# Kernel optimization log

Hardware: AMD Instinct MI355X
Metric: run time of the kernel (lower is better)

Reference implementation:

```python
import jax, jax.numpy as jnp
import numpy as np

N = 50000  # nodes
E = 1600000  # directed edges
F_IN = 64
H = 64
C = 16
EPS = 1e-12


def setup_inputs() -> dict:
    key = jax.random.key(0)
    ks = jax.random.split(key, 10)
    x = jax.random.normal(ks[0], (N, F_IN), jnp.float32)
    edge_index = jax.random.randint(ks[1], (2, E), 0, N, dtype=jnp.int32)
    def lin(k, fan_in, fan_out):
        return jax.random.normal(k, (fan_in, fan_out), jnp.float32) * (1.0 / np.sqrt(fan_in))
    return {
        "x": x,
        "edge_index": edge_index,
        "W1": lin(ks[2], F_IN, H), "b1": jnp.zeros((H,), jnp.float32),
        "W2": lin(ks[3], H, H),    "b2": jnp.zeros((H,), jnp.float32),
        "W3": lin(ks[4], H, H),    "b3": jnp.zeros((H,), jnp.float32),
        "Wlin": lin(ks[5], 3 * H, C), "blin": jnp.zeros((C,), jnp.float32),
    }


def _gcn_norm(edge_index, n):
    # add self loops, compute symmetric GCN normalization D^-1/2 (A+I) D^-1/2
    loop = jnp.arange(n, dtype=edge_index.dtype)
    row = jnp.concatenate([edge_index[0], loop])  # target nodes
    col = jnp.concatenate([edge_index[1], loop])  # source nodes
    deg = jax.ops.segment_sum(jnp.ones_like(row, dtype=jnp.float32), row, num_segments=n)
    dis = jnp.where(deg > 0, jax.lax.rsqrt(jnp.maximum(deg, 1.0)), 0.0)
    norm = dis[row] * dis[col]  # [E+N]
    return row, col, norm


def _gcn_layer(x, row, col, norm, W, b):
    h = x @ W                              # [N, H]
    msg = h[col] * norm[:, None]           # gather sources, scale
    agg = jax.ops.segment_sum(msg, row, num_segments=x.shape[0])  # scatter-add
    return agg + b


def _l2norm(x):
    # torch F.normalize(p=2, dim=1)
    n = jnp.sqrt(jnp.sum(x * x, axis=1, keepdims=True))
    return x / jnp.maximum(n, EPS)


def reference(x, edge_index, W1, b1, W2, b2, W3, b3, Wlin, blin):
    row, col, norm = _gcn_norm(edge_index, x.shape[0])
    stack = []
    h = x
    for (W, b) in ((W1, b1), (W2, b2), (W3, b3)):
        h = _gcn_layer(h, row, col, norm, W, b)
        h = jax.nn.relu(h)
        h = _l2norm(h)
        stack.append(h)
    emb = jnp.concatenate(stack, axis=1)   # [N, 3H]
    out = emb @ Wlin + blin                # [N, C]
    return jax.nn.log_softmax(out, axis=1)
```

## Files before the change

kernel.cpp:

```cpp
#include <hip/hip_runtime.h>
#include <hip/hip_bf16.h>

#define NN 50000
#define EE 1600000
#define NB 391
#define CAPB 4608
#define CPAD 16
#define EPB 4096
#define BCAP 28

typedef __attribute__((ext_vector_type(8))) short short8;
typedef __attribute__((ext_vector_type(4))) float floatx4;

__device__ __forceinline__ float ldext(const void* p, long i, int f32) {
    return f32 ? ((const float*)p)[i]
               : __bfloat162float(((const __hip_bfloat16*)p)[i]);
}

__device__ __forceinline__ float b2f(unsigned short u) {
    unsigned int x = ((unsigned int)u) << 16;
    float f; __builtin_memcpy(&f, &x, 4); return f;
}
__device__ __forceinline__ unsigned short f2b(float f) {
    __hip_bfloat16 h = __float2bfloat16(f);
    unsigned short u; __builtin_memcpy(&u, &h, 2); return u;
}
__device__ __forceinline__ float asf(unsigned int x) {
    float f; __builtin_memcpy(&f, &x, 4); return f;
}

__global__ void k_bucket(const int* __restrict__ row, const int* __restrict__ col,
                         int* __restrict__ bcur, unsigned int* __restrict__ bdata,
                         const unsigned short* __restrict__ xu, int* __restrict__ flag) {
    __shared__ int lcnt[NB];
    __shared__ unsigned binned[NB * BCAP];
    __shared__ int dcnt;
    int tid = threadIdx.x;
    if (blockIdx.x == 0) {
        if (tid == 0) dcnt = 0;
        __syncthreads();
        int local = 0;
        for (int j = 0; j < 16; ++j) {
            unsigned short u = xu[2 * (tid + 256 * j)];
            int ex = (u >> 7) & 0xFF;
            if (ex == 0xFF || ex < 0x60) local++;
        }
        atomicAdd(&dcnt, local);
        __syncthreads();
        if (tid == 0) flag[0] = (dcnt > 256) ? 1 : 0;
    }
    long base = (long)blockIdx.x * EPB;
    int nedge = (int)min((long)EPB, (long)EE - base);
    for (int k = tid; k < NB; k += 256) lcnt[k] = 0;
    __syncthreads();
    const int4* r4 = (const int4*)(row + base);
    const int4* c4 = (const int4*)(col + base);
    for (int j = tid; j < (nedge >> 2); j += 256) {
        int4 rr = r4[j], cc = c4[j];
        #pragma unroll
        for (int t = 0; t < 4; ++t) {
            int r = (&rr.x)[t], c = (&cc.x)[t];
            int b = r >> 7;
            unsigned rec = ((unsigned)(r & 127) << 16) | (unsigned)c;
            int p = atomicAdd(&lcnt[b], 1);
            if (p < BCAP) binned[b * BCAP + p] = rec;
            else {
                int gp = atomicAdd(&bcur[b * CPAD], 1);
                if (gp < CAPB) bdata[(long)b * CAPB + gp] = rec;
            }
        }
    }
    __syncthreads();
    for (int b = tid; b < NB; b += 256) {
        int n = min(lcnt[b], BCAP);
        if (!n) continue;
        int gb = atomicAdd(&bcur[b * CPAD], n);
        long dst = (long)b * CAPB;
        for (int j = 0; j < n; ++j)
            if (gb + j < CAPB) bdata[dst + gb + j] = binned[b * BCAP + j];
    }
}

__global__ void k_csr(const int* __restrict__ bcur, const unsigned* __restrict__ bdata,
                      int* __restrict__ row_ptr, float* __restrict__ dis,
                      unsigned short* __restrict__ csr_col) {
    __shared__ unsigned recs[CAPB];
    __shared__ int cnt[128];
    __shared__ int incl[128];
    __shared__ int curs[128];
    __shared__ int redu[4];
    int b = blockIdx.x, tid = threadIdx.x;
    int lane = tid & 63, wid = tid >> 6;
    int part = 0;
    for (int j = tid; j < b; j += 256) part += min(bcur[j * CPAD], CAPB);
    #pragma unroll
    for (int off = 32; off; off >>= 1) part += __shfl_xor(part, off);
    if (lane == 0) redu[wid] = part;
    if (tid < 128) cnt[tid] = 0;
    __syncthreads();
    int base = redu[0] + redu[1] + redu[2] + redu[3];
    int n = min(bcur[b * CPAD], CAPB);
    const unsigned* dp = bdata + (long)b * CAPB;
    for (int i = tid; i < n; i += 256) {
        unsigned rec = dp[i];
        recs[i] = rec;
        atomicAdd(&cnt[(rec >> 16) & 127], 1);
    }
    __syncthreads();
    if (tid < 128) {
        int x = cnt[tid];
        #pragma unroll
        for (int off = 1; off < 64; off <<= 1) {
            int y = __shfl_up(x, off);
            if (lane >= off) x += y;
        }
        incl[tid] = x;
    }
    __syncthreads();
    int r0 = b << 7;
    if (tid < 128) {
        int ic = incl[tid] + (wid == 1 ? incl[63] : 0);
        int excl = base + ic - cnt[tid];
        curs[tid] = excl;
        int r = r0 + tid;
        if (r <= NN) row_ptr[r] = excl;
        if (r < NN) dis[r] = rsqrtf((float)(cnt[tid] + 1));
    }
    __syncthreads();
    for (int i = tid; i < n; i += 256) {
        unsigned rec = recs[i];
        int p = atomicAdd(&curs[(rec >> 16) & 127], 1);
        csr_col[p] = (unsigned short)(rec & 0xFFFF);
    }
}

template <bool EXT>
__global__ void k_gemm(const void* __restrict__ X, const void* __restrict__ W,
                       const int* __restrict__ flag, const float* __restrict__ dis,
                       unsigned short* __restrict__ Hout) {
    __shared__ __align__(16) unsigned short xs[64 * 72];
    int tid = threadIdx.x;
    int n0 = blockIdx.x * 64;
    const int f32 = flag[0];
    for (int idx = tid; idx < 4096; idx += 256) {
        int nn = idx >> 6, k = idx & 63;
        int n = n0 + nn;
        unsigned short v = 0;
        if (n < NN) {
            long ofs = (long)n * 64 + k;
            if (EXT) v = f32 ? f2b(((const float*)X)[ofs]) : ((const unsigned short*)X)[ofs];
            else     v = ((const unsigned short*)X)[ofs];
        }
        xs[nn * 72 + k] = v;
    }
    __syncthreads();
    int lane = tid & 63, wid = tid >> 6;
    int m0 = wid * 16;
    int quad = lane >> 4, nl = lane & 15;
    short8 a0 = *(const short8*)(xs + (m0 + nl) * 72 + quad * 8);
    short8 a1 = *(const short8*)(xs + (m0 + nl) * 72 + quad * 8 + 32);
    floatx4 acc[4];
    const unsigned short* Wb = (const unsigned short*)W;
    const float* Wf = (const float*)W;
    #pragma unroll
    for (int ct = 0; ct < 4; ++ct) {
        short8 b0, b1;
        int n = ct * 16 + nl;
        #pragma unroll
        for (int j = 0; j < 8; ++j) {
            int k0 = quad * 8 + j;
            b0[j] = (short)(f32 ? f2b(Wf[k0 * 64 + n]) : Wb[k0 * 64 + n]);
            b1[j] = (short)(f32 ? f2b(Wf[(k0 + 32) * 64 + n]) : Wb[(k0 + 32) * 64 + n]);
        }
        floatx4 c = {0.f, 0.f, 0.f, 0.f};
        c = __builtin_amdgcn_mfma_f32_16x16x32_bf16(a0, b0, c, 0, 0, 0);
        c = __builtin_amdgcn_mfma_f32_16x16x32_bf16(a1, b1, c, 0, 0, 0);
        acc[ct] = c;
    }
    #pragma unroll
    for (int r = 0; r < 4; ++r) {
        int node = n0 + m0 + quad * 4 + r;
        if (node < NN) {
            float dn = dis[node];
            #pragma unroll
            for (int ct = 0; ct < 4; ++ct)
                Hout[(long)node * 64 + ct * 16 + nl] = f2b(dn * acc[ct][r]);
        }
    }
}

__global__ void k_agg(const uint4* __restrict__ hp128, const int* __restrict__ row_ptr,
                      const unsigned short* __restrict__ csr_col,
                      const float* __restrict__ dis, const void* __restrict__ bias,
                      const int* __restrict__ flag,
                      unsigned short* __restrict__ eo ) {
    int lane = threadIdx.x & 63, wid = threadIdx.x >> 6;
    int half = lane >> 5;
    int i = blockIdx.x * 8 + wid * 2 + half;
    bool valid = (i < NN);
    int iv = valid ? i : 0;
    int q4 = (lane >> 3) & 3;
    int fl = lane & 7;
    float2 A0 = {0,0}, A1 = {0,0}, A2 = {0,0}, A3 = {0,0};
    #define ADDU(u) do { \
        A0.x += asf((u).x << 16); A0.y += asf((u).x & 0xFFFF0000u); \
        A1.x += asf((u).y << 16); A1.y += asf((u).y & 0xFFFF0000u); \
        A2.x += asf((u).z << 16); A2.y += asf((u).z & 0xFFFF0000u); \
        A3.x += asf((u).w << 16); A3.y += asf((u).w & 0xFFFF0000u); } while (0)
    if (valid && q4 == 0) {
        uint4 u = hp128[(long)iv * 8 + fl];
        ADDU(u);
    }
    int e  = valid ? row_ptr[iv] : 0;
    int e1 = valid ? row_ptr[iv + 1] : 0;
    while (e + 15 < e1) {
        int c0 = csr_col[e + q4];
        int c1 = csr_col[e + 4 + q4];
        int c2 = csr_col[e + 8 + q4];
        int c3 = csr_col[e + 12 + q4];
        uint4 u0 = hp128[(long)c0 * 8 + fl];
        uint4 u1 = hp128[(long)c1 * 8 + fl];
        uint4 u2 = hp128[(long)c2 * 8 + fl];
        uint4 u3 = hp128[(long)c3 * 8 + fl];
        ADDU(u0); ADDU(u1); ADDU(u2); ADDU(u3);
        e += 16;
    }
    if (e + 7 < e1) {
        int c0 = csr_col[e + q4];
        int c1 = csr_col[e + 4 + q4];
        uint4 u0 = hp128[(long)c0 * 8 + fl];
        uint4 u1 = hp128[(long)c1 * 8 + fl];
        ADDU(u0); ADDU(u1);
        e += 8;
    }
    if (e + 3 < e1) {
        int c = csr_col[e + q4];
        uint4 u = hp128[(long)c * 8 + fl];
        ADDU(u);
        e += 4;
    }
    int rem = e1 - e;
    if (q4 < rem) {
        int c = csr_col[e + q4];
        uint4 u = hp128[(long)c * 8 + fl];
        ADDU(u);
    }
    #undef ADDU
    #pragma unroll
    for (int off = 8; off < 32; off <<= 1) {
        A0.x += __shfl_xor(A0.x, off); A0.y += __shfl_xor(A0.y, off);
        A1.x += __shfl_xor(A1.x, off); A1.y += __shfl_xor(A1.y, off);
        A2.x += __shfl_xor(A2.x, off); A2.y += __shfl_xor(A2.y, off);
        A3.x += __shfl_xor(A3.x, off); A3.y += __shfl_xor(A3.y, off);
    }
    const int f32 = flag[0];
    float di = dis[iv];
    float v0 = fmaf(di, A0.x, ldext(bias, 8 * fl + 0, f32));
    float v1 = fmaf(di, A0.y, ldext(bias, 8 * fl + 1, f32));
    float v2 = fmaf(di, A1.x, ldext(bias, 8 * fl + 2, f32));
    float v3 = fmaf(di, A1.y, ldext(bias, 8 * fl + 3, f32));
    float v4 = fmaf(di, A2.x, ldext(bias, 8 * fl + 4, f32));
    float v5 = fmaf(di, A2.y, ldext(bias, 8 * fl + 5, f32));
    float v6 = fmaf(di, A3.x, ldext(bias, 8 * fl + 6, f32));
    float v7 = fmaf(di, A3.y, ldext(bias, 8 * fl + 7, f32));
    v0 = fmaxf(v0, 0.f); v1 = fmaxf(v1, 0.f); v2 = fmaxf(v2, 0.f); v3 = fmaxf(v3, 0.f);
    v4 = fmaxf(v4, 0.f); v5 = fmaxf(v5, 0.f); v6 = fmaxf(v6, 0.f); v7 = fmaxf(v7, 0.f);
    float s = fmaf(v0, v0, fmaf(v1, v1, fmaf(v2, v2, v3 * v3)))
            + fmaf(v4, v4, fmaf(v5, v5, fmaf(v6, v6, v7 * v7)));
    #pragma unroll
    for (int off = 4; off; off >>= 1) s += __shfl_xor(s, off);
    float inv = 1.f / fmaxf(sqrtf(s), 1e-12f);
    if (valid && q4 == 0) {
        union { unsigned short us[8]; uint4 v; } pk;
        pk.us[0] = f2b(v0 * inv); pk.us[1] = f2b(v1 * inv);
        pk.us[2] = f2b(v2 * inv); pk.us[3] = f2b(v3 * inv);
        pk.us[4] = f2b(v4 * inv); pk.us[5] = f2b(v5 * inv);
        pk.us[6] = f2b(v6 * inv); pk.us[7] = f2b(v7 * inv);
        *(uint4*)(eo + (long)i * 64 + 8 * fl) = pk.v;
    }
}

__global__ void k_out(const unsigned short* __restrict__ emb, const void* __restrict__ Wlin,
                      const void* __restrict__ blin, const int* __restrict__ flag,
                      void* __restrict__ out) {
    int tid = threadIdx.x, lane = tid & 63, wid = tid >> 6;
    int quad = lane >> 4, nl = lane & 15;
    int base = blockIdx.x * 64 + wid * 16;
    const int f32 = flag[0];
    const unsigned short* Wb = (const unsigned short*)Wlin;
    const float* Wf = (const float*)Wlin;
    int ia = min(base + nl, NN - 1);
    floatx4 c = {0.f, 0.f, 0.f, 0.f};
    #pragma unroll
    for (int kc = 0; kc < 6; ++kc) {
        short8 b;
        #pragma unroll
        for (int j = 0; j < 8; ++j) {
            int k = kc * 32 + quad * 8 + j;
            b[j] = (short)(f32 ? f2b(Wf[k * 16 + nl]) : Wb[k * 16 + nl]);
        }
        int L = kc >> 1, ko = (kc & 1) * 32 + quad * 8;
        short8 a = *(const short8*)(emb + (long)L * NN * 64 + (long)ia * 64 + ko);
        c = __builtin_amdgcn_mfma_f32_16x16x32_bf16(a, b, c, 0, 0, 0);
    }
    float bl = ldext(blin, nl, f32);
    #pragma unroll
    for (int r = 0; r < 4; ++r) {
        float v = c[r] + bl;
        float m = v;
        #pragma unroll
        for (int off = 1; off < 16; off <<= 1) m = fmaxf(m, __shfl_xor(m, off));
        float ex = __expf(v - m);
        float s = ex;
        #pragma unroll
        for (int off = 1; off < 16; off <<= 1) s += __shfl_xor(s, off);
        float o = (v - m) - __logf(s);
        int node = base + quad * 4 + r;
        if (node < NN) {
            long oidx = (long)node * 16 + nl;
            if (f32) ((float*)out)[oidx] = o;
            else     ((__hip_bfloat16*)out)[oidx] = __float2bfloat16(o);
        }
    }
}

extern "C" void kernel_launch(void* const* d_in, const int* in_sizes, int n_in,
                              void* d_out, int out_size, void* d_ws, size_t ws_size,
                              hipStream_t stream) {
    const void* x    = d_in[0];
    const int*  ei   = (const int*)d_in[1];
    const void* W1   = d_in[2];
    const void* b1   = d_in[3];
    const void* W2   = d_in[4];
    const void* b2   = d_in[5];
    const void* W3   = d_in[6];
    const void* b3   = d_in[7];
    const void* Wlin = d_in[8];
    const void* blin = d_in[9];

    unsigned short* h   = (unsigned short*)d_ws;
    unsigned short* emb = h + (long)NN * 64;
    float* dis     = (float*)(emb + (long)3 * NN * 64);
    int*   row_ptr = (int*)(dis + NN);
    int*   flag    = row_ptr + NN + 64;
    int*   bcur    = flag + 16;
    unsigned* bdata = (unsigned*)(bcur + NB * CPAD);
    unsigned short* csr_col = (unsigned short*)(bdata + (long)NB * CAPB);

    const int* row = ei;
    const int* col = ei + EE;

    (void)hipMemsetAsync(bcur, 0, NB * CPAD * sizeof(int), stream);
    k_bucket<<<(EE + EPB - 1) / EPB, 256, 0, stream>>>(row, col, bcur, bdata,
                                                       (const unsigned short*)x, flag);
    k_csr<<<NB, 256, 0, stream>>>(bcur, bdata, row_ptr, dis, csr_col);

    int gb = (NN + 63) / 64;
    int ga = (NN + 7) / 8;
    const uint4* hp128 = (const uint4*)h;
    k_gemm<true><<<gb, 256, 0, stream>>>(x, W1, flag, dis, h);
    k_agg<<<ga, 256, 0, stream>>>(hp128, row_ptr, csr_col, dis, b1, flag, emb);
    k_gemm<false><<<gb, 256, 0, stream>>>(emb, W2, flag, dis, h);
    k_agg<<<ga, 256, 0, stream>>>(hp128, row_ptr, csr_col, dis, b2, flag, emb + (long)NN * 64);
    k_gemm<false><<<gb, 256, 0, stream>>>(emb + (long)NN * 64, W3, flag, dis, h);
    k_agg<<<ga, 256, 0, stream>>>(hp128, row_ptr, csr_col, dis, b3, flag, emb + (long)2 * NN * 64);

    k_out<<<gb, 256, 0, stream>>>(emb, Wlin, blin, flag, d_out);
}
```

Before: 286.6 us.

## Slice hidden features into 8-column planes and defer L2 normalization downstream

Stores the hidden matrix as eight feature slices of 8 bf16 each, so each aggregation block handles one slice and its gathers touch a 800KB plane that can stay cache-resident, with 32 lanes striding over edges per node. L2 normalization moves out of aggregation: each slice writes its partial sum of squares, and the next GEMM or the output kernel combines them and applies the inverse norm. This cuts the gather working set but multiplies block count by 8 and re-reads row_ptr and csr_col once per slice. It also relies on NN being divisible by 8, since the grid drops the bounds check.

```diff
diff --git a/kernel.cpp b/kernel.cpp
--- a/kernel.cpp
+++ b/kernel.cpp
@@ -135,21 +135,37 @@
 }
 
 template <bool EXT>
-__global__ void k_gemm(const void* __restrict__ X, const void* __restrict__ W,
-                       const int* __restrict__ flag, const float* __restrict__ dis,
-                       unsigned short* __restrict__ Hout) {
+__global__ void k_gemm(const void* __restrict__ X, const float* __restrict__ sqin,
+                       const void* __restrict__ W, const int* __restrict__ flag,
+                       const float* __restrict__ dis,
+                       unsigned short* __restrict__ hs) {
     __shared__ __align__(16) unsigned short xs[64 * 72];
+    __shared__ float inv[64];
     int tid = threadIdx.x;
     int n0 = blockIdx.x * 64;
     const int f32 = flag[0];
+    if (!EXT) {
+        if (tid < 64) {
+            int node = min(n0 + tid, NN - 1);
+            float s8 = 0.f;
+            #pragma unroll
+            for (int s = 0; s < 8; ++s) s8 += sqin[(long)s * NN + node];
+            inv[tid] = 1.f / fmaxf(sqrtf(s8), 1e-12f);
+        }
+        __syncthreads();
+    }
     for (int idx = tid; idx < 4096; idx += 256) {
         int nn = idx >> 6, k = idx & 63;
         int n = n0 + nn;
         unsigned short v = 0;
         if (n < NN) {
-            long ofs = (long)n * 64 + k;
-            if (EXT) v = f32 ? f2b(((const float*)X)[ofs]) : ((const unsigned short*)X)[ofs];
-            else     v = ((const unsigned short*)X)[ofs];
+            if (EXT) {
+                long ofs = (long)n * 64 + k;
+                v = f32 ? f2b(((const float*)X)[ofs]) : ((const unsigned short*)X)[ofs];
+            } else {
+                unsigned short tv = ((const unsigned short*)X)[((long)(k >> 3) * NN + n) * 8 + (k & 7)];
+                v = f2b(b2f(tv) * inv[nn]);
+            }
         }
         xs[nn * 72 + k] = v;
     }
@@ -183,114 +199,91 @@
         if (node < NN) {
             float dn = dis[node];
             #pragma unroll
-            for (int ct = 0; ct < 4; ++ct)
-                Hout[(long)node * 64 + ct * 16 + nl] = f2b(dn * acc[ct][r]);
-        }
-    }
-}
-
-__global__ void k_agg(const uint4* __restrict__ hp128, const int* __restrict__ row_ptr,
+            for (int ct = 0; ct < 4; ++ct) {
+                int slice = 2 * ct + (nl >> 3);
+                hs[((long)slice * NN + node) * 8 + (nl & 7)] = f2b(dn * acc[ct][r]);
+            }
+        }
+    }
+}
+
+__global__ void k_agg(const uint4* __restrict__ hs, const int* __restrict__ row_ptr,
                       const unsigned short* __restrict__ csr_col,
                       const float* __restrict__ dis, const void* __restrict__ bias,
                       const int* __restrict__ flag,
-                      unsigned short* __restrict__ eo ) {
+                      unsigned short* __restrict__ t, float* __restrict__ sq) {
     int lane = threadIdx.x & 63, wid = threadIdx.x >> 6;
-    int half = lane >> 5;
-    int i = blockIdx.x * 8 + wid * 2 + half;
-    bool valid = (i < NN);
-    int iv = valid ? i : 0;
-    int q4 = (lane >> 3) & 3;
-    int fl = lane & 7;
+    int s = blockIdx.x & 7;
+    int half = lane >> 5, el = lane & 31;
+    int i = (blockIdx.x >> 3) * 8 + wid * 2 + half;
+    const uint4* hss = hs + (long)s * NN;
     float2 A0 = {0,0}, A1 = {0,0}, A2 = {0,0}, A3 = {0,0};
     #define ADDU(u) do { \
         A0.x += asf((u).x << 16); A0.y += asf((u).x & 0xFFFF0000u); \
         A1.x += asf((u).y << 16); A1.y += asf((u).y & 0xFFFF0000u); \
         A2.x += asf((u).z << 16); A2.y += asf((u).z & 0xFFFF0000u); \
         A3.x += asf((u).w << 16); A3.y += asf((u).w & 0xFFFF0000u); } while (0)
-    if (valid && q4 == 0) {
-        uint4 u = hp128[(long)iv * 8 + fl];
+    if (el == 0) {
+        uint4 u = hss[i];
         ADDU(u);
     }
-    int e  = valid ? row_ptr[iv] : 0;
-    int e1 = valid ? row_ptr[iv + 1] : 0;
-    while (e + 15 < e1) {
-        int c0 = csr_col[e + q4];
-        int c1 = csr_col[e + 4 + q4];
-        int c2 = csr_col[e + 8 + q4];
-        int c3 = csr_col[e + 12 + q4];
-        uint4 u0 = hp128[(long)c0 * 8 + fl];
-        uint4 u1 = hp128[(long)c1 * 8 + fl];
-        uint4 u2 = hp128[(long)c2 * 8 + fl];
-        uint4 u3 = hp128[(long)c3 * 8 + fl];
-        ADDU(u0); ADDU(u1); ADDU(u2); ADDU(u3);
-        e += 16;
-    }
-    if (e + 7 < e1) {
-        int c0 = csr_col[e + q4];
-        int c1 = csr_col[e + 4 + q4];
-        uint4 u0 = hp128[(long)c0 * 8 + fl];
-        uint4 u1 = hp128[(long)c1 * 8 + fl];
-        ADDU(u0); ADDU(u1);
-        e += 8;
-    }
-    if (e + 3 < e1) {
-        int c = csr_col[e + q4];
-        uint4 u = hp128[(long)c * 8 + fl];
+    int e0 = row_ptr[i], e1 = row_ptr[i + 1];
+    for (int e = e0 + el; e < e1; e += 32) {
+        int c = csr_col[e];
+        uint4 u = hss[c];
         ADDU(u);
-        e += 4;
-    }
-    int rem = e1 - e;
-    if (q4 < rem) {
-        int c = csr_col[e + q4];
-        uint4 u = hp128[(long)c * 8 + fl];
-        ADDU(u);
     }
     #undef ADDU
     #pragma unroll
-    for (int off = 8; off < 32; off <<= 1) {
+    for (int off = 1; off < 32; off <<= 1) {
         A0.x += __shfl_xor(A0.x, off); A0.y += __shfl_xor(A0.y, off);
         A1.x += __shfl_xor(A1.x, off); A1.y += __shfl_xor(A1.y, off);
         A2.x += __shfl_xor(A2.x, off); A2.y += __shfl_xor(A2.y, off);
         A3.x += __shfl_xor(A3.x, off); A3.y += __shfl_xor(A3.y, off);
     }
     const int f32 = flag[0];
-    float di = dis[iv];
-    float v0 = fmaf(di, A0.x, ldext(bias, 8 * fl + 0, f32));
-    float v1 = fmaf(di, A0.y, ldext(bias, 8 * fl + 1, f32));
-    float v2 = fmaf(di, A1.x, ldext(bias, 8 * fl + 2, f32));
-    float v3 = fmaf(di, A1.y, ldext(bias, 8 * fl + 3, f32));
-    float v4 = fmaf(di, A2.x, ldext(bias, 8 * fl + 4, f32));
-    float v5 = fmaf(di, A2.y, ldext(bias, 8 * fl + 5, f32));
-    float v6 = fmaf(di, A3.x, ldext(bias, 8 * fl + 6, f32));
-    float v7 = fmaf(di, A3.y, ldext(bias, 8 * fl + 7, f32));
-    v0 = fmaxf(v0, 0.f); v1 = fmaxf(v1, 0.f); v2 = fmaxf(v2, 0.f); v3 = fmaxf(v3, 0.f);
-    v4 = fmaxf(v4, 0.f); v5 = fmaxf(v5, 0.f); v6 = fmaxf(v6, 0.f); v7 = fmaxf(v7, 0.f);
-    float s = fmaf(v0, v0, fmaf(v1, v1, fmaf(v2, v2, v3 * v3)))
-            + fmaf(v4, v4, fmaf(v5, v5, fmaf(v6, v6, v7 * v7)));
-    #pragma unroll
-    for (int off = 4; off; off >>= 1) s += __shfl_xor(s, off);
-    float inv = 1.f / fmaxf(sqrtf(s), 1e-12f);
-    if (valid && q4 == 0) {
+    float di = dis[i];
+    float v0 = fmaxf(fmaf(di, A0.x, ldext(bias, 8 * s + 0, f32)), 0.f);
+    float v1 = fmaxf(fmaf(di, A0.y, ldext(bias, 8 * s + 1, f32)), 0.f);
+    float v2 = fmaxf(fmaf(di, A1.x, ldext(bias, 8 * s + 2, f32)), 0.f);
+    float v3 = fmaxf(fmaf(di, A1.y, ldext(bias, 8 * s + 3, f32)), 0.f);
+    float v4 = fmaxf(fmaf(di, A2.x, ldext(bias, 8 * s + 4, f32)), 0.f);
+    float v5 = fmaxf(fmaf(di, A2.y, ldext(bias, 8 * s + 5, f32)), 0.f);
+    float v6 = fmaxf(fmaf(di, A3.x, ldext(bias, 8 * s + 6, f32)), 0.f);
+    float v7 = fmaxf(fmaf(di, A3.y, ldext(bias, 8 * s + 7, f32)), 0.f);
+    if (el == 0) {
+        float ss = fmaf(v0, v0, fmaf(v1, v1, fmaf(v2, v2, v3 * v3)))
+                 + fmaf(v4, v4, fmaf(v5, v5, fmaf(v6, v6, v7 * v7)));
         union { unsigned short us[8]; uint4 v; } pk;
-        pk.us[0] = f2b(v0 * inv); pk.us[1] = f2b(v1 * inv);
-        pk.us[2] = f2b(v2 * inv); pk.us[3] = f2b(v3 * inv);
-        pk.us[4] = f2b(v4 * inv); pk.us[5] = f2b(v5 * inv);
-        pk.us[6] = f2b(v6 * inv); pk.us[7] = f2b(v7 * inv);
-        *(uint4*)(eo + (long)i * 64 + 8 * fl) = pk.v;
-    }
-}
-
-__global__ void k_out(const unsigned short* __restrict__ emb, const void* __restrict__ Wlin,
-                      const void* __restrict__ blin, const int* __restrict__ flag,
-                      void* __restrict__ out) {
+        pk.us[0] = f2b(v0); pk.us[1] = f2b(v1); pk.us[2] = f2b(v2); pk.us[3] = f2b(v3);
+        pk.us[4] = f2b(v4); pk.us[5] = f2b(v5); pk.us[6] = f2b(v6); pk.us[7] = f2b(v7);
+        *(uint4*)(t + ((long)s * NN + i) * 8) = pk.v;
+        sq[(long)s * NN + i] = ss;
+    }
+}
+
+__global__ void k_out(const unsigned short* __restrict__ t, const float* __restrict__ sq,
+                      const void* __restrict__ Wlin, const void* __restrict__ blin,
+                      const int* __restrict__ flag, void* __restrict__ out) {
+    __shared__ float invs[3][64];
     int tid = threadIdx.x, lane = tid & 63, wid = tid >> 6;
     int quad = lane >> 4, nl = lane & 15;
-    int base = blockIdx.x * 64 + wid * 16;
+    int base64 = blockIdx.x * 64;
+    int base = base64 + wid * 16;
     const int f32 = flag[0];
+    if (tid < 192) {
+        int L = tid >> 6, j = tid & 63;
+        int node = min(base64 + j, NN - 1);
+        float s8 = 0.f;
+        #pragma unroll
+        for (int s = 0; s < 8; ++s) s8 += sq[(long)L * NN * 8 + (long)s * NN + node];
+        invs[L][j] = 1.f / fmaxf(sqrtf(s8), 1e-12f);
+    }
+    __syncthreads();
     const unsigned short* Wb = (const unsigned short*)Wlin;
     const float* Wf = (const float*)Wlin;
     int ia = min(base + nl, NN - 1);
-    floatx4 c = {0.f, 0.f, 0.f, 0.f};
+    floatx4 c[3] = {{0,0,0,0}, {0,0,0,0}, {0,0,0,0}};
     #pragma unroll
     for (int kc = 0; kc < 6; ++kc) {
         short8 b;
@@ -300,22 +293,24 @@
             b[j] = (short)(f32 ? f2b(Wf[k * 16 + nl]) : Wb[k * 16 + nl]);
         }
         int L = kc >> 1, ko = (kc & 1) * 32 + quad * 8;
-        short8 a = *(const short8*)(emb + (long)L * NN * 64 + (long)ia * 64 + ko);
-        c = __builtin_amdgcn_mfma_f32_16x16x32_bf16(a, b, c, 0, 0, 0);
+        short8 a = *(const short8*)(t + (long)L * NN * 64 + ((long)(ko >> 3) * NN + ia) * 8);
+        c[L] = __builtin_amdgcn_mfma_f32_16x16x32_bf16(a, b, c[L], 0, 0, 0);
     }
     float bl = ldext(blin, nl, f32);
     #pragma unroll
     for (int r = 0; r < 4; ++r) {
-        float v = c[r] + bl;
+        int nloc = wid * 16 + quad * 4 + r;
+        float v = c[0][r] * invs[0][nloc] + c[1][r] * invs[1][nloc]
+                + c[2][r] * invs[2][nloc] + bl;
         float m = v;
         #pragma unroll
         for (int off = 1; off < 16; off <<= 1) m = fmaxf(m, __shfl_xor(m, off));
         float ex = __expf(v - m);
-        float s = ex;
-        #pragma unroll
-        for (int off = 1; off < 16; off <<= 1) s += __shfl_xor(s, off);
-        float o = (v - m) - __logf(s);
-        int node = base + quad * 4 + r;
+        float sm = ex;
+        #pragma unroll
+        for (int off = 1; off < 16; off <<= 1) sm += __shfl_xor(sm, off);
+        float o = (v - m) - __logf(sm);
+        int node = base64 + nloc;
         if (node < NN) {
             long oidx = (long)node * 16 + nl;
             if (f32) ((float*)out)[oidx] = o;
@@ -338,9 +333,10 @@
     const void* Wlin = d_in[8];
     const void* blin = d_in[9];
 
-    unsigned short* h   = (unsigned short*)d_ws;
-    unsigned short* emb = h + (long)NN * 64;
-    float* dis     = (float*)(emb + (long)3 * NN * 64);
+    unsigned short* hs  = (unsigned short*)d_ws;
+    unsigned short* t   = hs + (long)NN * 64;
+    float* sq      = (float*)(t + (long)3 * NN * 64);
+    float* dis     = sq + (long)3 * NN * 8;
     int*   row_ptr = (int*)(dis + NN);
     int*   flag    = row_ptr + NN + 64;
     int*   bcur    = flag + 16;
@@ -356,14 +352,18 @@
     k_csr<<<NB, 256, 0, stream>>>(bcur, bdata, row_ptr, dis, csr_col);
 
     int gb = (NN + 63) / 64;
-    int ga = (NN + 7) / 8;
-    const uint4* hp128 = (const uint4*)h;
-    k_gemm<true><<<gb, 256, 0, stream>>>(x, W1, flag, dis, h);
-    k_agg<<<ga, 256, 0, stream>>>(hp128, row_ptr, csr_col, dis, b1, flag, emb);
-    k_gemm<false><<<gb, 256, 0, stream>>>(emb, W2, flag, dis, h);
-    k_agg<<<ga, 256, 0, stream>>>(hp128, row_ptr, csr_col, dis, b2, flag, emb + (long)NN * 64);
-    k_gemm<false><<<gb, 256, 0, stream>>>(emb + (long)NN * 64, W3, flag, dis, h);
-    k_agg<<<ga, 256, 0, stream>>>(hp128, row_ptr, csr_col, dis, b3, flag, emb + (long)2 * NN * 64);
-
-    k_out<<<gb, 256, 0, stream>>>(emb, Wlin, blin, flag, d_out);
-}
+    int ga = (NN / 8) * 8;
+    const uint4* hs128 = (const uint4*)hs;
+    k_gemm<true><<<gb, 256, 0, stream>>>(x, nullptr, W1, flag, dis, hs);
+    k_agg<<<ga, 256, 0, stream>>>(hs128, row_ptr, csr_col, dis, b1, flag,
+                                  t, sq);
+    k_gemm<false><<<gb, 256, 0, stream>>>(t, sq, W2, flag, dis, hs);
+    k_agg<<<ga, 256, 0, stream>>>(hs128, row_ptr, csr_col, dis, b2, flag,
+                                  t + (long)NN * 64, sq + (long)NN * 8);
+    k_gemm<false><<<gb, 256, 0, stream>>>(t + (long)NN * 64, sq + (long)NN * 8,
+                                          W3, flag, dis, hs);
+    k_agg<<<ga, 256, 0, stream>>>(hs128, row_ptr, csr_col, dis, b3, flag,
+                                  t + (long)2 * NN * 64, sq + (long)2 * NN * 8);
+
+    k_out<<<gb, 256, 0, stream>>>(t, sq, Wlin, blin, flag, d_out);
+}
```

Result: slower. 452.9 us (+58.0%).
